# Kernel tuning notes

Hardware: AMD Instinct MI355X
Metric: run time of the kernel (lower is better)

Reference implementation:

```python
import jax, jax.numpy as jnp
import numpy as np
from jax import lax

RADIUS = 0.2
K = 32
EPS = 1e-5  # torch BatchNorm default eps

B, N, M, C = 16, 4096, 1024, 64


def setup_inputs() -> dict:
    key = jax.random.key(0)
    ks = jax.random.split(key, 8)
    src_x = jax.random.normal(ks[0], (B, N, C), dtype=jnp.float32)
    src_xyz = jax.random.uniform(ks[1], (B, N, 3), dtype=jnp.float32)
    xyz = jax.random.uniform(ks[2], (B, M, 3), dtype=jnp.float32)
    w1 = jax.random.normal(ks[3], (64, C + 3), dtype=jnp.float32) * 0.05
    w2 = jax.random.normal(ks[4], (128, 64), dtype=jnp.float32) * 0.05
    w3 = jax.random.normal(ks[5], (256, 128), dtype=jnp.float32) * 0.05
    return {
        "src_x": src_x, "src_xyz": src_xyz, "xyz": xyz,
        "w1": w1, "g1": jnp.ones(64), "b1": jnp.zeros(64),
        "w2": w2, "g2": jnp.ones(128), "b2": jnp.zeros(128),
        "w3": w3, "gl": jnp.ones(256), "bl": jnp.zeros(256),
    }


def _ball_query(src_xyz, xyz):
    # squared distances [B, M, N]
    d2 = jnp.sum((xyz[:, :, None, :] - src_xyz[:, None, :, :]) ** 2, axis=-1)
    n = src_xyz.shape[1]
    col = jnp.arange(n, dtype=jnp.int32)
    # encode: in-ball points keep their index, others get sentinel n
    score = jnp.where(d2 <= RADIUS * RADIUS, col, n)
    neg_top, _ = lax.top_k(-score, K)        # k smallest scores (first-k in index order)
    gidx = -neg_top                          # [B, M, K]
    first = gidx[..., :1]
    first = jnp.where(first >= n, 0, first)  # no neighbor at all -> 0 (degenerate)
    gidx = jnp.where(gidx >= n, first, gidx)  # pad slots repeat first neighbor
    return gidx


def _gather(src, gidx):
    # src [B, N, D], gidx [B, M, K] -> [B, M, K, D]
    b, m, k = gidx.shape
    out = jnp.take_along_axis(src, gidx.reshape(b, m * k, 1), axis=1)
    return out.reshape(b, m, k, src.shape[-1])


def _bn(x, g, b, axes):
    # training-mode batch norm over given axes, per last-dim channel (biased var)
    mean = jnp.mean(x, axis=axes, keepdims=True)
    var = jnp.mean((x - mean) ** 2, axis=axes, keepdims=True)
    return (x - mean) * lax.rsqrt(var + EPS) * g + b


def _gelu(x):
    return jax.nn.gelu(x, approximate=False)  # torch nn.GELU default (erf)


def reference(src_x, src_xyz, xyz, w1, g1, b1, w2, g2, b2, w3, gl, bl):
    gidx = _ball_query(src_xyz, xyz)                 # [B, M, K]
    grouped_xyz = _gather(src_xyz, gidx)             # [B, M, K, 3]
    centered = grouped_xyz - xyz[:, :, None, :]
    grouped_x = _gather(src_x, gidx)                 # [B, M, K, C]
    feat = jnp.concatenate([centered, grouped_x], axis=-1)  # [B, M, K, C+3]

    h = _gelu(_bn(jnp.einsum("bmkc,oc->bmko", feat, w1), g1, b1, (0, 1, 2)))
    h = _gelu(_bn(jnp.einsum("bmkc,oc->bmko", h, w2), g2, b2, (0, 1, 2)))
    h = jnp.einsum("bmkc,oc->bmko", h, w3)
    h = jnp.max(h, axis=2)                           # max over k neighbors -> [B, M, 256]
    return _gelu(_bn(h, gl, bl, (0, 1)))             # BatchNorm1d over (batch, points)
```

## Files before the change

kernel.cpp:

```cpp
#include <hip/hip_runtime.h>
#include <math.h>

#define BB 16
#define NN 4096
#define MM 1024
#define KNN 32
#define R2 0.04f
#define EPSV 1e-5f
#define S1f ((float)(BB * MM * KNN))
#define S3f ((float)(BB * MM))

typedef __attribute__((ext_vector_type(8))) short short8;
typedef __attribute__((ext_vector_type(4))) short short4v;
typedef __attribute__((ext_vector_type(4))) float f32x4;

__device__ __forceinline__ short f2b(float x) {
    union { float f; unsigned u; } v; v.f = x;
    unsigned r = v.u + 0x7fffu + ((v.u >> 16) & 1u);
    return (short)(r >> 16);
}
__device__ __forceinline__ float b2f(short s) {
    union { unsigned u; float f; } v; v.u = ((unsigned)(unsigned short)s) << 16;
    return v.f;
}
__device__ __forceinline__ float gelu_t(float x) {
    float u = 0.7978845608f * x * (1.f + 0.044715f * x * x);
    float e = __expf(2.f * u);
    float r = __builtin_amdgcn_rcpf(e + 1.f);
    return x - x * r;
}
__device__ __forceinline__ float gelu_e(float x) {
    return 0.5f * x * (1.f + erff(x * 0.7071067811865475f));
}
__device__ __forceinline__ f32x4 zero4() { f32x4 z = {0.f, 0.f, 0.f, 0.f}; return z; }
__device__ __forceinline__ f32x4 mfma(short8 a, short8 b, f32x4 c) {
    return __builtin_amdgcn_mfma_f32_16x16x32_bf16(a, b, c, 0, 0, 0);
}
__device__ __forceinline__ short8 pack8(f32x4 a, f32x4 b) {
    short8 r;
    r[0] = f2b(a[0]); r[1] = f2b(a[1]); r[2] = f2b(a[2]); r[3] = f2b(a[3]);
    r[4] = f2b(b[0]); r[5] = f2b(b[1]); r[6] = f2b(b[2]); r[7] = f2b(b[3]);
    return r;
}

__global__ __launch_bounds__(256) void k_ballquery(const float* __restrict__ src_xyz,
                                                   const float* __restrict__ xyz,
                                                   int* __restrict__ gidx) {
    __shared__ float sx[NN], sy[NN], sz[NN];
    int t = threadIdx.x;
    int lane = t & 63, w = t >> 6;
    int q0 = blockIdx.x * 16;
    int b = q0 >> 10;
    const float* sp = src_xyz + (size_t)b * NN * 3;
    for (int i = t; i < NN * 3; i += 256) {
        float v = sp[i];
        int j = i / 3, d = i - j * 3;
        if (d == 0) sx[j] = v;
        else if (d == 1) sy[j] = v;
        else sz[j] = v;
    }
    __syncthreads();
#pragma unroll
    for (int qi = 0; qi < 4; ++qi) {
        int q = q0 + w * 4 + qi;
        int m = q & 1023;
        float qx = xyz[((size_t)b * MM + m) * 3 + 0];
        float qy = xyz[((size_t)b * MM + m) * 3 + 1];
        float qz = xyz[((size_t)b * MM + m) * 3 + 2];
        int* outp = gidx + (size_t)q * KNN;
        int cnt = 0, firstj = -1;
        for (int j0 = 0; j0 < NN && cnt < KNN; j0 += 64) {
            int j = j0 + lane;
            float dx = qx - sx[j];
            float dy = qy - sy[j];
            float dz = qz - sz[j];
            bool hit = (dx * dx + dy * dy + dz * dz) <= R2;
            unsigned long long mask = __ballot(hit);
            if (hit) {
                int rank = cnt + __popcll(mask & ((1ull << lane) - 1ull));
                if (rank < KNN) outp[rank] = j;
            }
            if (firstj < 0 && mask != 0ull) firstj = j0 + __ffsll((long long)mask) - 1;
            cnt += __popcll(mask);
        }
        if (cnt < KNN) {
            int fj = (firstj < 0) ? 0 : firstj;
            for (int k = cnt + lane; k < KNN; k += 64) outp[k] = fj;
        }
    }
}

__global__ __launch_bounds__(256) void k_prep(const float* __restrict__ src_x,
                                              const float* __restrict__ w1,
                                              const float* __restrict__ w2,
                                              const float* __restrict__ w3,
                                              short* __restrict__ src_xb,
                                              short* __restrict__ w1b,
                                              short* __restrict__ w2b,
                                              short* __restrict__ w3b,
                                              short* __restrict__ w3p) {
    int i = blockIdx.x * 256 + threadIdx.x;
    if (i < 524288) {
        const f32x4* p = (const f32x4*)(src_x + (size_t)i * 8);
        *(short8*)(src_xb + (size_t)i * 8) = pack8(p[0], p[1]);
    } else {
        int j = i - 524288;
        if (j < 6144) {
            int n = j / 96, k = j % 96;
            float v = 0.f;
            if (k < 64) v = w1[n * 67 + 3 + k];
            else if (k < 67) v = w1[n * 67 + (k - 64)];
            w1b[j] = f2b(v);
        } else if (j < 14336) {
            w2b[j - 6144] = f2b(w2[j - 6144]);
        } else if (j < 47104) {
            w3b[j - 14336] = f2b(w3[j - 14336]);
        } else if (j < 79872) {
            int j2 = j - 47104;
            int e = j2 & 7;
            int lane = (j2 >> 3) & 63;
            int idx = j2 >> 9;
            int nf = idx & 3, kf = (idx >> 2) & 3, nc = idx >> 4;
            int ln = lane & 15, qq = lane >> 4;
            w3p[j2] = f2b(w3[(size_t)(nc * 64 + nf * 16 + ln) * 128 + kf * 32 + qq * 8 + e]);
        }
    }
}

#define GATHER_WAVE(R)                                                                  \
    {                                                                                   \
        if (lane < 8) { short4v z4 = {0, 0, 0, 0};                                      \
            *(short4v*)((R) + 2304 + lane * 4) = z4; }                                  \
        int r = lane >> 1, hf = lane & 1;                                               \
        int jdx = gidx[(size_t)g * KNN + r];                                            \
        const short8* sp = (const short8*)(src_xb + ((size_t)b * NN + jdx) * 64 + hf * 32); \
        *(short8*)((R) + r * 72 + hf * 32) = sp[0];                                     \
        *(short8*)((R) + r * 72 + hf * 32 + 8) = sp[1];                                 \
        *(short8*)((R) + r * 72 + hf * 32 + 16) = sp[2];                                \
        *(short8*)((R) + r * 72 + hf * 32 + 24) = sp[3];                                \
        if (hf == 0) {                                                                  \
            const float* spp = src_xyz + ((size_t)b * NN + jdx) * 3;                    \
            short4v z;                                                                  \
            z[0] = f2b(spp[0] - qx); z[1] = f2b(spp[1] - qy);                           \
            z[2] = f2b(spp[2] - qz); z[3] = 0;                                          \
            *(short4v*)((R) + r * 72 + 64) = z;                                         \
            short4v z0 = {0, 0, 0, 0};                                                  \
            *(short4v*)((R) + r * 72 + 68) = z0;                                        \
        }                                                                               \
    }

#define BN1_SCALES                                                                      \
    if (t < 64) {                                                                       \
        float s = 0.f, sq = 0.f;                                                        \
        _Pragma("unroll")                                                               \
        for (int r = 0; r < 8; ++r) { s += stats1[r * 128 + t]; sq += stats1[r * 128 + 64 + t]; } \
        float mu = s * (1.f / S1f);                                                     \
        float var = sq * (1.f / S1f) - mu * mu;                                         \
        float rs = rsqrtf(var + EPSV);                                                  \
        float sc = g1[t] * rs;                                                          \
        sc1L[t] = sc;                                                                   \
        sh1L[t] = b1[t] - mu * sc;                                                      \
    }

#define L1_SWAPPED(R, acc1)                                                             \
    short8 bAct[2][3];                                                                  \
    _Pragma("unroll")                                                                   \
    for (int sf = 0; sf < 2; ++sf)                                                      \
        _Pragma("unroll")                                                               \
        for (int kf = 0; kf < 3; ++kf)                                                  \
            bAct[sf][kf] = *(const short8*)((R) + (sf * 16 + ln) * 72 + kf * 32 + qq * 8); \
    _Pragma("unroll")                                                                   \
    for (int sf = 0; sf < 2; ++sf)                                                      \
        _Pragma("unroll")                                                               \
        for (int nf = 0; nf < 4; ++nf) acc1[sf][nf] = zero4();                          \
    _Pragma("unroll")                                                                   \
    for (int kf = 0; kf < 3; ++kf)                                                      \
        _Pragma("unroll")                                                               \
        for (int nf = 0; nf < 4; ++nf) {                                                \
            short8 aW = *(const short8*)(w1b + (nf * 16 + ln) * 96 + kf * 32 + qq * 8); \
            acc1[0][nf] = mfma(aW, bAct[0][kf], acc1[0][nf]);                           \
            acc1[1][nf] = mfma(aW, bAct[1][kf], acc1[1][nf]);                           \
        }

__global__ __launch_bounds__(256, 6) void k_s1(const int* __restrict__ gidx,
                                               const float* __restrict__ src_xyz,
                                               const float* __restrict__ xyz,
                                               const short* __restrict__ src_xb,
                                               const short* __restrict__ w1b,
                                               float* __restrict__ stats1) {
    __shared__ short wbuf[4][2336];
    __shared__ float redS[256], redQ[256];
    int t = threadIdx.x, lane = t & 63, w = t >> 6, ln = lane & 15, qq = lane >> 4;
    int g = blockIdx.x * 4 + w, b = g >> 10, m = g & 1023;
    float qx = xyz[((size_t)b * MM + m) * 3 + 0];
    float qy = xyz[((size_t)b * MM + m) * 3 + 1];
    float qz = xyz[((size_t)b * MM + m) * 3 + 2];
    short* R = wbuf[w];
    GATHER_WAVE(R)
    f32x4 acc1[2][4];
    L1_SWAPPED(R, acc1)
#pragma unroll
    for (int nf = 0; nf < 4; ++nf) {
        f32x4 s, q;
#pragma unroll
        for (int jj = 0; jj < 4; ++jj) {
            float a0 = acc1[0][nf][jj], a1 = acc1[1][nf][jj];
            s[jj] = a0 + a1; q[jj] = a0 * a0 + a1 * a1;
        }
#pragma unroll
        for (int d = 1; d < 16; d <<= 1) {
#pragma unroll
            for (int jj = 0; jj < 4; ++jj) {
                s[jj] += __shfl_xor(s[jj], d);
                q[jj] += __shfl_xor(q[jj], d);
            }
        }
        if (ln == 0) {
            *(f32x4*)(redS + w * 64 + nf * 16 + qq * 4) = s;
            *(f32x4*)(redQ + w * 64 + nf * 16 + qq * 4) = q;
        }
    }
    __syncthreads();
    if (t < 64) {
        float s = redS[t] + redS[64 + t] + redS[128 + t] + redS[192 + t];
        float q = redQ[t] + redQ[64 + t] + redQ[128 + t] + redQ[192 + t];
        float* st = stats1 + (blockIdx.x & 7) * 128;
        atomicAdd(&st[t], s);
        atomicAdd(&st[64 + t], q);
    }
}

__global__ __launch_bounds__(256, 4) void k_s2(const int* __restrict__ gidx,
                                               const float* __restrict__ src_xyz,
                                               const float* __restrict__ xyz,
                                               const short* __restrict__ src_xb,
                                               const short* __restrict__ w1b,
                                               const short* __restrict__ w2b,
                                               const float* __restrict__ g1,
                                               const float* __restrict__ b1,
                                               const float* __restrict__ stats1,
                                               float* __restrict__ stats2,
                                               short* __restrict__ h2p) {
    __shared__ short wbuf[4][2336];
    __shared__ float sc1L[64], sh1L[64];
    __shared__ float redS[512], redQ[512];
    int t = threadIdx.x, lane = t & 63, w = t >> 6, ln = lane & 15, qq = lane >> 4;
    int g = blockIdx.x * 4 + w, b = g >> 10, m = g & 1023;
    float qx = xyz[((size_t)b * MM + m) * 3 + 0];
    float qy = xyz[((size_t)b * MM + m) * 3 + 1];
    float qz = xyz[((size_t)b * MM + m) * 3 + 2];
    short* R = wbuf[w];
    GATHER_WAVE(R)
    BN1_SCALES
    f32x4 acc1[2][4];
    L1_SWAPPED(R, acc1)
    __syncthreads();
#pragma unroll
    for (int sf = 0; sf < 2; ++sf)
#pragma unroll
        for (int nf = 0; nf < 4; ++nf) {
            int c0 = nf * 16 + qq * 4;
            f32x4 sc = *(const f32x4*)(sc1L + c0);
            f32x4 sh = *(const f32x4*)(sh1L + c0);
            short4v sv;
#pragma unroll
            for (int jj = 0; jj < 4; ++jj)
                sv[jj] = f2b(gelu_t(acc1[sf][nf][jj] * sc[jj] + sh[jj]));
            *(short4v*)(R + (sf * 16 + ln) * 72 + c0) = sv;
        }
    short8 bh1[2][2];
#pragma unroll
    for (int sf = 0; sf < 2; ++sf)
#pragma unroll
        for (int kf = 0; kf < 2; ++kf)
            bh1[sf][kf] = *(const short8*)(R + (sf * 16 + ln) * 72 + kf * 32 + qq * 8);
    f32x4 acc2[2][8];
#pragma unroll
    for (int sf = 0; sf < 2; ++sf)
#pragma unroll
        for (int nf = 0; nf < 8; ++nf) acc2[sf][nf] = zero4();
#pragma unroll
    for (int kf = 0; kf < 2; ++kf)
#pragma unroll
        for (int nf = 0; nf < 8; ++nf) {
            short8 aW = *(const short8*)(w2b + (nf * 16 + ln) * 64 + kf * 32 + qq * 8);
            acc2[0][nf] = mfma(aW, bh1[0][kf], acc2[0][nf]);
            acc2[1][nf] = mfma(aW, bh1[1][kf], acc2[1][nf]);
        }
    {
        short* hb = h2p + (size_t)g * 4096;
#pragma unroll
        for (int i = 0; i < 8; ++i) {
            int sf = i >> 2, p = i & 3;
            *(short8*)(hb + (i * 64 + lane) * 8) = pack8(acc2[sf][2 * p], acc2[sf][2 * p + 1]);
        }
    }
#pragma unroll
    for (int nf = 0; nf < 8; ++nf) {
        f32x4 s, q;
#pragma unroll
        for (int jj = 0; jj < 4; ++jj) {
            float a0 = acc2[0][nf][jj], a1 = acc2[1][nf][jj];
            s[jj] = a0 + a1; q[jj] = a0 * a0 + a1 * a1;
        }
#pragma unroll
        for (int d = 1; d < 16; d <<= 1) {
#pragma unroll
            for (int jj = 0; jj < 4; ++jj) {
                s[jj] += __shfl_xor(s[jj], d);
                q[jj] += __shfl_xor(q[jj], d);
            }
        }
        if (ln == 0) {
            *(f32x4*)(redS + w * 128 + nf * 16 + qq * 4) = s;
            *(f32x4*)(redQ + w * 128 + nf * 16 + qq * 4) = q;
        }
    }
    __syncthreads();
    if (t < 128) {
        float s = redS[t] + redS[128 + t] + redS[256 + t] + redS[384 + t];
        float q = redQ[t] + redQ[128 + t] + redQ[256 + t] + redQ[384 + t];
        float* st = stats2 + (blockIdx.x & 7) * 256;
        atomicAdd(&st[t], s);
        atomicAdd(&st[128 + t], q);
    }
}

__global__ __launch_bounds__(256, 4) void k3(const short* __restrict__ h2p,
                                             const short* __restrict__ w3p,
                                             const float* __restrict__ g2,
                                             const float* __restrict__ b2,
                                             const float* __restrict__ stats2,
                                             float* __restrict__ out) {
    __shared__ short wbuf[4][4352];
    __shared__ float sc2L[128], sh2L[128];
    int t = threadIdx.x, lane = t & 63, w = t >> 6, ln = lane & 15, qq = lane >> 4;
    int g = blockIdx.x * 4 + w;
    const short* hb = h2p + (size_t)g * 4096;
    short8 hv[8];
#pragma unroll
    for (int i = 0; i < 8; ++i) hv[i] = *(const short8*)(hb + (i * 64 + lane) * 8);
    if (t < 128) {
        float s = 0.f, sq = 0.f;
#pragma unroll
        for (int r = 0; r < 8; ++r) { s += stats2[r * 256 + t]; sq += stats2[r * 256 + 128 + t]; }
        float mu = s * (1.f / S1f);
        float var = sq * (1.f / S1f) - mu * mu;
        float rs = rsqrtf(var + EPSV);
        float sc = g2[t] * rs;
        sc2L[t] = sc;
        sh2L[t] = b2[t] - mu * sc;
    }
    __syncthreads();
    short* R = wbuf[w];
#pragma unroll
    for (int i = 0; i < 8; ++i) {
        int sf = i >> 2, p = i & 3;
#pragma unroll
        for (int hh = 0; hh < 2; ++hh) {
            int c0 = (2 * p + hh) * 16 + qq * 4;
            f32x4 sc = *(const f32x4*)(sc2L + c0);
            f32x4 sh = *(const f32x4*)(sh2L + c0);
            short4v sv;
#pragma unroll
            for (int jj = 0; jj < 4; ++jj)
                sv[jj] = f2b(gelu_t(b2f(hv[i][hh * 4 + jj]) * sc[jj] + sh[jj]));
            *(short4v*)(R + (sf * 16 + ln) * 136 + c0) = sv;
        }
    }
    short8 b3[2][4];
#pragma unroll
    for (int sf = 0; sf < 2; ++sf)
#pragma unroll
        for (int kf = 0; kf < 4; ++kf)
            b3[sf][kf] = *(const short8*)(R + (sf * 16 + ln) * 136 + kf * 32 + qq * 8);
#pragma unroll
    for (int nc = 0; nc < 4; ++nc) {
        f32x4 acc3[2][4];
#pragma unroll
        for (int sf = 0; sf < 2; ++sf)
#pragma unroll
            for (int nf = 0; nf < 4; ++nf) acc3[sf][nf] = zero4();
#pragma unroll
        for (int kf = 0; kf < 4; ++kf)
#pragma unroll
            for (int nf = 0; nf < 4; ++nf) {
                short8 aW = *(const short8*)(w3p + (((nc * 4 + kf) * 4 + nf) * 64 + lane) * 8);
                acc3[0][nf] = mfma(aW, b3[0][kf], acc3[0][nf]);
                acc3[1][nf] = mfma(aW, b3[1][kf], acc3[1][nf]);
            }
#pragma unroll
        for (int nf = 0; nf < 4; ++nf) {
            f32x4 v;
#pragma unroll
            for (int jj = 0; jj < 4; ++jj) v[jj] = fmaxf(acc3[0][nf][jj], acc3[1][nf][jj]);
#pragma unroll
            for (int d = 1; d < 16; d <<= 1) {
#pragma unroll
                for (int jj = 0; jj < 4; ++jj) v[jj] = fmaxf(v[jj], __shfl_xor(v[jj], d));
            }
            if (ln == 0)
                *(f32x4*)(out + (size_t)g * 256 + nc * 64 + nf * 16 + qq * 4) = v;
        }
    }
}

__global__ __launch_bounds__(256) void k_stats3(const float* __restrict__ out,
                                                float* __restrict__ stats3) {
    int t = threadIdx.x;
    float s = 0.f, q = 0.f;
    const float* p = out + (size_t)blockIdx.x * 128 * 256 + t;
    for (int r = 0; r < 128; ++r) { float v = p[r * 256]; s += v; q += v * v; }
    atomicAdd(&stats3[t], s);
    atomicAdd(&stats3[256 + t], q);
}

__global__ __launch_bounds__(256) void k_bn3(float* __restrict__ out,
                                             const float* __restrict__ stats3,
                                             const float* __restrict__ gl,
                                             const float* __restrict__ bl) {
    int i = blockIdx.x * 256 + threadIdx.x;
    int o = i & 255;
    float mu = stats3[o] * (1.f / S3f);
    float var = stats3[256 + o] * (1.f / S3f) - mu * mu;
    float rs = rsqrtf(var + EPSV);
    float x = out[i];
    out[i] = gelu_e((x - mu) * rs * gl[o] + bl[o]);
}

extern "C" void kernel_launch(void* const* d_in, const int* in_sizes, int n_in,
                              void* d_out, int out_size, void* d_ws, size_t ws_size,
                              hipStream_t stream) {
    const float* src_x   = (const float*)d_in[0];
    const float* src_xyz = (const float*)d_in[1];
    const float* xyz     = (const float*)d_in[2];
    const float* w1      = (const float*)d_in[3];
    const float* g1      = (const float*)d_in[4];
    const float* b1      = (const float*)d_in[5];
    const float* w2      = (const float*)d_in[6];
    const float* g2      = (const float*)d_in[7];
    const float* b2      = (const float*)d_in[8];
    const float* w3      = (const float*)d_in[9];
    const float* gl      = (const float*)d_in[10];
    const float* bl      = (const float*)d_in[11];
    float* out = (float*)d_out;

    int* gidx = (int*)d_ws;
    float* statsF = (float*)(gidx + BB * MM * KNN);
    float* stats1 = statsF;
    float* stats2 = statsF + 1024;
    float* stats3 = statsF + 3072;
    short* wb = (short*)(statsF + 3584);
    short* w1b = wb;
    short* w2b = wb + 6144;
    short* w3b = wb + 14336;
    short* w3p = wb + 47104;
    short* src_xb = wb + 79872;
    short* h2p = (short*)((char*)d_ws + (size_t)(16u << 20));

    hipMemsetAsync(statsF, 0, 3584 * sizeof(float), stream);
    k_prep<<<2360, 256, 0, stream>>>(src_x, w1, w2, w3, src_xb, w1b, w2b, w3b, w3p);
    k_ballquery<<<(BB * MM) / 16, 256, 0, stream>>>(src_xyz, xyz, gidx);
    k_s1<<<(BB * MM) / 4, 256, 0, stream>>>(gidx, src_xyz, xyz, src_xb, w1b, stats1);
    k_s2<<<(BB * MM) / 4, 256, 0, stream>>>(gidx, src_xyz, xyz, src_xb, w1b, w2b, g1, b1,
                                            stats1, stats2, h2p);
    k3<<<(BB * MM) / 4, 256, 0, stream>>>(h2p, w3p, g2, b2, stats2, out);
    k_stats3<<<(BB * MM) / 128, 256, 0, stream>>>(out, stats3);
    k_bn3<<<BB * MM, 256, 0, stream>>>(out, stats3, gl, bl);
}
```

Measured before the change: 271.9 us.

## Materialize layer-1 activations to skip regather in stage 2; fuse BN3 stats

Stage 1 now writes its pre-BN layer-1 outputs as bf16 to a workspace buffer, and a new stage-2 kernel reads them back instead of redoing the gather and the first matmul. This runs only when the workspace is large enough; otherwise the old recompute path is used. The layer-3 statistics are also reduced inside k3 into 8 partial slots, which removes the separate k_stats3 pass over the output, and k_bn3 sums those slots. In exchange it adds about 64MB of extra write and read traffic, and the new path depends on the workspace size.

```diff
diff --git a/kernel.cpp b/kernel.cpp
--- a/kernel.cpp
+++ b/kernel.cpp
@@ -182,12 +182,88 @@
             acc1[1][nf] = mfma(aW, bAct[1][kf], acc1[1][nf]);                           \
         }
 
+#define H1_DECODE(R, hv)                                                                \
+    _Pragma("unroll")                                                                   \
+    for (int i = 0; i < 4; ++i) {                                                       \
+        int sf_ = i >> 1, pr_ = i & 1;                                                  \
+        _Pragma("unroll")                                                               \
+        for (int hh = 0; hh < 2; ++hh) {                                                \
+            int c0_ = (2 * pr_ + hh) * 16 + qq * 4;                                     \
+            f32x4 sc = *(const f32x4*)(sc1L + c0_);                                     \
+            f32x4 sh = *(const f32x4*)(sh1L + c0_);                                     \
+            short4v sv;                                                                 \
+            _Pragma("unroll")                                                           \
+            for (int jj = 0; jj < 4; ++jj)                                              \
+                sv[jj] = f2b(gelu_t(b2f(hv[i][hh * 4 + jj]) * sc[jj] + sh[jj]));        \
+            *(short4v*)((R) + (sf_ * 16 + ln) * 72 + c0_) = sv;                         \
+        }                                                                               \
+    }
+
+#define L2_TAIL(R)                                                                      \
+    short8 bh1[2][2];                                                                   \
+    _Pragma("unroll")                                                                   \
+    for (int sf = 0; sf < 2; ++sf)                                                      \
+        _Pragma("unroll")                                                               \
+        for (int kf = 0; kf < 2; ++kf)                                                  \
+            bh1[sf][kf] = *(const short8*)((R) + (sf * 16 + ln) * 72 + kf * 32 + qq * 8); \
+    f32x4 acc2[2][8];                                                                   \
+    _Pragma("unroll")                                                                   \
+    for (int sf = 0; sf < 2; ++sf)                                                      \
+        _Pragma("unroll")                                                               \
+        for (int nf = 0; nf < 8; ++nf) acc2[sf][nf] = zero4();                          \
+    _Pragma("unroll")                                                                   \
+    for (int kf = 0; kf < 2; ++kf)                                                      \
+        _Pragma("unroll")                                                               \
+        for (int nf = 0; nf < 8; ++nf) {                                                \
+            short8 aW = *(const short8*)(w2b + (nf * 16 + ln) * 64 + kf * 32 + qq * 8); \
+            acc2[0][nf] = mfma(aW, bh1[0][kf], acc2[0][nf]);                            \
+            acc2[1][nf] = mfma(aW, bh1[1][kf], acc2[1][nf]);                            \
+        }                                                                               \
+    {                                                                                   \
+        short* hb2 = h2p + (size_t)g * 4096;                                            \
+        _Pragma("unroll")                                                               \
+        for (int i = 0; i < 8; ++i) {                                                   \
+            int sf = i >> 2, p = i & 3;                                                 \
+            *(short8*)(hb2 + (i * 64 + lane) * 8) = pack8(acc2[sf][2 * p], acc2[sf][2 * p + 1]); \
+        }                                                                               \
+    }                                                                                   \
+    _Pragma("unroll")                                                                   \
+    for (int nf = 0; nf < 8; ++nf) {                                                    \
+        f32x4 s, q;                                                                     \
+        _Pragma("unroll")                                                               \
+        for (int jj = 0; jj < 4; ++jj) {                                                \
+            float a0 = acc2[0][nf][jj], a1 = acc2[1][nf][jj];                           \
+            s[jj] = a0 + a1; q[jj] = a0 * a0 + a1 * a1;                                 \
+        }                                                                               \
+        _Pragma("unroll")                                                               \
+        for (int d = 1; d < 16; d <<= 1) {                                              \
+            _Pragma("unroll")                                                           \
+            for (int jj = 0; jj < 4; ++jj) {                                            \
+                s[jj] += __shfl_xor(s[jj], d);                                          \
+                q[jj] += __shfl_xor(q[jj], d);                                          \
+            }                                                                           \
+        }                                                                               \
+        if (ln == 0) {                                                                  \
+            *(f32x4*)(redS + w * 128 + nf * 16 + qq * 4) = s;                           \
+            *(f32x4*)(redQ + w * 128 + nf * 16 + qq * 4) = q;                           \
+        }                                                                               \
+    }                                                                                   \
+    __syncthreads();                                                                    \
+    if (t < 128) {                                                                      \
+        float s = redS[t] + redS[128 + t] + redS[256 + t] + redS[384 + t];              \
+        float q = redQ[t] + redQ[128 + t] + redQ[256 + t] + redQ[384 + t];              \
+        float* st = stats2 + (blockIdx.x & 7) * 256;                                    \
+        atomicAdd(&st[t], s);                                                           \
+        atomicAdd(&st[128 + t], q);                                                     \
+    }
+
 __global__ __launch_bounds__(256, 6) void k_s1(const int* __restrict__ gidx,
                                                const float* __restrict__ src_xyz,
                                                const float* __restrict__ xyz,
                                                const short* __restrict__ src_xb,
                                                const short* __restrict__ w1b,
-                                               float* __restrict__ stats1) {
+                                               float* __restrict__ stats1,
+                                               short* __restrict__ h1p) {
     __shared__ short wbuf[4][2336];
     __shared__ float redS[256], redQ[256];
     int t = threadIdx.x, lane = t & 63, w = t >> 6, ln = lane & 15, qq = lane >> 4;
@@ -199,6 +275,14 @@
     GATHER_WAVE(R)
     f32x4 acc1[2][4];
     L1_SWAPPED(R, acc1)
+    if (h1p) {
+        short* hb = h1p + (size_t)g * 2048;
+#pragma unroll
+        for (int i = 0; i < 4; ++i) {
+            int sf = i >> 1, p = i & 1;
+            *(short8*)(hb + (i * 64 + lane) * 8) = pack8(acc1[sf][2 * p], acc1[sf][2 * p + 1]);
+        }
+    }
 #pragma unroll
     for (int nf = 0; nf < 4; ++nf) {
         f32x4 s, q;
@@ -228,6 +312,29 @@
         atomicAdd(&st[t], s);
         atomicAdd(&st[64 + t], q);
     }
+}
+
+__global__ __launch_bounds__(256, 6) void k_s2f(const short* __restrict__ h1p,
+                                                const short* __restrict__ w2b,
+                                                const float* __restrict__ g1,
+                                                const float* __restrict__ b1,
+                                                const float* __restrict__ stats1,
+                                                float* __restrict__ stats2,
+                                                short* __restrict__ h2p) {
+    __shared__ short wbuf[4][2336];
+    __shared__ float sc1L[64], sh1L[64];
+    __shared__ float redS[512], redQ[512];
+    int t = threadIdx.x, lane = t & 63, w = t >> 6, ln = lane & 15, qq = lane >> 4;
+    int g = blockIdx.x * 4 + w;
+    const short* hb = h1p + (size_t)g * 2048;
+    short8 hv[4];
+#pragma unroll
+    for (int i = 0; i < 4; ++i) hv[i] = *(const short8*)(hb + (i * 64 + lane) * 8);
+    BN1_SCALES
+    __syncthreads();
+    short* R = wbuf[w];
+    H1_DECODE(R, hv)
+    L2_TAIL(R)
 }
 
 __global__ __launch_bounds__(256, 4) void k_s2(const int* __restrict__ gidx,
@@ -268,62 +375,7 @@
                 sv[jj] = f2b(gelu_t(acc1[sf][nf][jj] * sc[jj] + sh[jj]));
             *(short4v*)(R + (sf * 16 + ln) * 72 + c0) = sv;
         }
-    short8 bh1[2][2];
-#pragma unroll
-    for (int sf = 0; sf < 2; ++sf)
-#pragma unroll
-        for (int kf = 0; kf < 2; ++kf)
-            bh1[sf][kf] = *(const short8*)(R + (sf * 16 + ln) * 72 + kf * 32 + qq * 8);
-    f32x4 acc2[2][8];
-#pragma unroll
-    for (int sf = 0; sf < 2; ++sf)
-#pragma unroll
-        for (int nf = 0; nf < 8; ++nf) acc2[sf][nf] = zero4();
-#pragma unroll
-    for (int kf = 0; kf < 2; ++kf)
-#pragma unroll
-        for (int nf = 0; nf < 8; ++nf) {
-            short8 aW = *(const short8*)(w2b + (nf * 16 + ln) * 64 + kf * 32 + qq * 8);
-            acc2[0][nf] = mfma(aW, bh1[0][kf], acc2[0][nf]);
-            acc2[1][nf] = mfma(aW, bh1[1][kf], acc2[1][nf]);
-        }
-    {
-        short* hb = h2p + (size_t)g * 4096;
-#pragma unroll
-        for (int i = 0; i < 8; ++i) {
-            int sf = i >> 2, p = i & 3;
-            *(short8*)(hb + (i * 64 + lane) * 8) = pack8(acc2[sf][2 * p], acc2[sf][2 * p + 1]);
-        }
-    }
-#pragma unroll
-    for (int nf = 0; nf < 8; ++nf) {
-        f32x4 s, q;
-#pragma unroll
-        for (int jj = 0; jj < 4; ++jj) {
-            float a0 = acc2[0][nf][jj], a1 = acc2[1][nf][jj];
-            s[jj] = a0 + a1; q[jj] = a0 * a0 + a1 * a1;
-        }
-#pragma unroll
-        for (int d = 1; d < 16; d <<= 1) {
-#pragma unroll
-            for (int jj = 0; jj < 4; ++jj) {
-                s[jj] += __shfl_xor(s[jj], d);
-                q[jj] += __shfl_xor(q[jj], d);
-            }
-        }
-        if (ln == 0) {
-            *(f32x4*)(redS + w * 128 + nf * 16 + qq * 4) = s;
-            *(f32x4*)(redQ + w * 128 + nf * 16 + qq * 4) = q;
-        }
-    }
-    __syncthreads();
-    if (t < 128) {
-        float s = redS[t] + redS[128 + t] + redS[256 + t] + redS[384 + t];
-        float q = redQ[t] + redQ[128 + t] + redQ[256 + t] + redQ[384 + t];
-        float* st = stats2 + (blockIdx.x & 7) * 256;
-        atomicAdd(&st[t], s);
-        atomicAdd(&st[128 + t], q);
-    }
+    L2_TAIL(R)
 }
 
 __global__ __launch_bounds__(256, 4) void k3(const short* __restrict__ h2p,
@@ -331,9 +383,11 @@
                                              const float* __restrict__ g2,
                                              const float* __restrict__ b2,
                                              const float* __restrict__ stats2,
+                                             float* __restrict__ stats3,
                                              float* __restrict__ out) {
     __shared__ short wbuf[4][4352];
     __shared__ float sc2L[128], sh2L[128];
+    __shared__ float mxS[4][256];
     int t = threadIdx.x, lane = t & 63, w = t >> 6, ln = lane & 15, qq = lane >> 4;
     int g = blockIdx.x * 4 + w;
     const short* hb = h2p + (size_t)g * 4096;
@@ -399,20 +453,21 @@
 #pragma unroll
                 for (int jj = 0; jj < 4; ++jj) v[jj] = fmaxf(v[jj], __shfl_xor(v[jj], d));
             }
-            if (ln == 0)
+            if (ln == 0) {
                 *(f32x4*)(out + (size_t)g * 256 + nc * 64 + nf * 16 + qq * 4) = v;
-        }
-    }
-}
-
-__global__ __launch_bounds__(256) void k_stats3(const float* __restrict__ out,
-                                                float* __restrict__ stats3) {
-    int t = threadIdx.x;
-    float s = 0.f, q = 0.f;
-    const float* p = out + (size_t)blockIdx.x * 128 * 256 + t;
-    for (int r = 0; r < 128; ++r) { float v = p[r * 256]; s += v; q += v * v; }
-    atomicAdd(&stats3[t], s);
-    atomicAdd(&stats3[256 + t], q);
+                *(f32x4*)(&mxS[w][nc * 64 + nf * 16 + qq * 4]) = v;
+            }
+        }
+    }
+    __syncthreads();
+    if (t < 256) {
+        float a0 = mxS[0][t], a1 = mxS[1][t], a2 = mxS[2][t], a3 = mxS[3][t];
+        float s = a0 + a1 + a2 + a3;
+        float q = a0 * a0 + a1 * a1 + a2 * a2 + a3 * a3;
+        float* st = stats3 + (blockIdx.x & 7) * 512;
+        atomicAdd(&st[t], s);
+        atomicAdd(&st[256 + t], q);
+    }
 }
 
 __global__ __launch_bounds__(256) void k_bn3(float* __restrict__ out,
@@ -421,8 +476,11 @@
                                              const float* __restrict__ bl) {
     int i = blockIdx.x * 256 + threadIdx.x;
     int o = i & 255;
-    float mu = stats3[o] * (1.f / S3f);
-    float var = stats3[256 + o] * (1.f / S3f) - mu * mu;
+    float s = 0.f, q = 0.f;
+#pragma unroll
+    for (int r = 0; r < 8; ++r) { s += stats3[r * 512 + o]; q += stats3[r * 512 + 256 + o]; }
+    float mu = s * (1.f / S3f);
+    float var = q * (1.f / S3f) - mu * mu;
     float rs = rsqrtf(var + EPSV);
     float x = out[i];
     out[i] = gelu_e((x - mu) * rs * gl[o] + bl[o]);
@@ -450,21 +508,29 @@
     float* stats1 = statsF;
     float* stats2 = statsF + 1024;
     float* stats3 = statsF + 3072;
-    short* wb = (short*)(statsF + 3584);
+    short* wb = (short*)(statsF + 7168);
     short* w1b = wb;
     short* w2b = wb + 6144;
     short* w3b = wb + 14336;
     short* w3p = wb + 47104;
     short* src_xb = wb + 79872;
-    short* h2p = (short*)((char*)d_ws + (size_t)(16u << 20));
-
-    hipMemsetAsync(statsF, 0, 3584 * sizeof(float), stream);
+    short* h1p = (short*)((char*)d_ws + (size_t)(16u << 20));
+    const size_t NEED_BIG = (size_t)(208u) << 20;
+    bool big = ws_size >= NEED_BIG;
+    short* h2p = big ? (short*)((char*)d_ws + ((size_t)(80u) << 20))
+                     : (short*)((char*)d_ws + ((size_t)(16u) << 20));
+
+    hipMemsetAsync(statsF, 0, 7168 * sizeof(float), stream);
     k_prep<<<2360, 256, 0, stream>>>(src_x, w1, w2, w3, src_xb, w1b, w2b, w3b, w3p);
     k_ballquery<<<(BB * MM) / 16, 256, 0, stream>>>(src_xyz, xyz, gidx);
-    k_s1<<<(BB * MM) / 4, 256, 0, stream>>>(gidx, src_xyz, xyz, src_xb, w1b, stats1);
-    k_s2<<<(BB * MM) / 4, 256, 0, stream>>>(gidx, src_xyz, xyz, src_xb, w1b, w2b, g1, b1,
-                                            stats1, stats2, h2p);
-    k3<<<(BB * MM) / 4, 256, 0, stream>>>(h2p, w3p, g2, b2, stats2, out);
-    k_stats3<<<(BB * MM) / 128, 256, 0, stream>>>(out, stats3);
+    k_s1<<<(BB * MM) / 4, 256, 0, stream>>>(gidx, src_xyz, xyz, src_xb, w1b, stats1,
+                                            big ? h1p : (short*)nullptr);
+    if (big) {
+        k_s2f<<<(BB * MM) / 4, 256, 0, stream>>>(h1p, w2b, g1, b1, stats1, stats2, h2p);
+    } else {
+        k_s2<<<(BB * MM) / 4, 256, 0, stream>>>(gidx, src_xyz, xyz, src_xb, w1b, w2b, g1, b1,
+                                                stats1, stats2, h2p);
+    }
+    k3<<<(BB * MM) / 4, 256, 0, stream>>>(h2p, w3p, g2, b2, stats2, stats3, out);
     k_bn3<<<BB * MM, 256, 0, stream>>>(out, stats3, gl, bl);
 }
```

After: 312.2 us. +14.8%, slower.
